# Optimization experiments

Hardware: AMD Instinct MI355X
Metric: run time of the kernel (lower is better)

## Reference

```python
import jax, jax.numpy as jnp
import numpy as np

N = 50000
E = 800000
D = 128
L = 2


def setup_inputs() -> dict:
    key = jax.random.key(0)
    ks = jax.random.split(key, 8)
    x = jax.random.normal(ks[0], (N, D), dtype=jnp.float32)
    edge_index = jax.random.randint(ks[1], (2, E), 0, N, dtype=jnp.int64)
    s = 1.0 / np.sqrt(D)
    Wl = jax.random.uniform(ks[2], (L, D, D), jnp.float32, -s, s)  # neighbor transform (with bias)
    bl = jax.random.uniform(ks[3], (L, D), jnp.float32, -s, s)
    Wr = jax.random.uniform(ks[4], (L, D, D), jnp.float32, -s, s)  # root/self transform (no bias)
    W = jax.random.uniform(ks[5], (D, D), jnp.float32, -s, s)      # final Linear
    b = jax.random.uniform(ks[6], (D,), jnp.float32, -s, s)
    return {"x": x, "edge_index": edge_index, "Wl": Wl, "bl": bl, "Wr": Wr, "W": W, "b": b}


def reference(x, edge_index, Wl, bl, Wr, W, b):
    src, dst = edge_index[0], edge_index[1]
    n = x.shape[0]
    for l in range(Wl.shape[0]):
        # gather neighbor (source) features, scatter-max into destination nodes
        agg = jax.ops.segment_max(x[src], dst, num_segments=n)  # [N, D]
        agg = jnp.where(jnp.isneginf(agg), 0.0, agg)  # PyG: isolated nodes -> 0
        # SAGEConv: lin_l(agg) + lin_r(x)
        x = agg @ Wl[l].T + bl[l] + x @ Wr[l].T
        x = jax.nn.relu(x)
    return x @ W.T + b
```

## Files before the change

### kernel.cpp

```cpp
#include <hip/hip_runtime.h>
#include <math.h>

#define NN 50000
#define NE 800000
#define DD 128
#define NBUCK 196
#define PTILE 4096
#define PBLOCKS 196
#define CONVB 6250

typedef unsigned short u16;
typedef short s8v __attribute__((ext_vector_type(8)));
typedef float f16v __attribute__((ext_vector_type(16)));

__device__ __forceinline__ u16 f2bf(float f) {
    unsigned u = __float_as_uint(f);
    return (u16)((u + 0x7FFFu + ((u >> 16) & 1u)) >> 16);
}
__device__ __forceinline__ float bflo(unsigned u) { return __uint_as_float(u << 16); }
__device__ __forceinline__ float bfhi(unsigned u) { return __uint_as_float(u & 0xFFFF0000u); }

__device__ __forceinline__ void pack_one(const float* __restrict__ Wl,
                                         const float* __restrict__ Wr,
                                         bool two, int o, u16* __restrict__ out) {
    int j = o & 7;
    int l = (o >> 3) & 63;
    int cn = o >> 9;
    int n = cn & 3;
    int c = cn >> 2;
    int colj = n * 32 + (l & 31);
    int k = c * 16 + (l >> 5) * 8 + j;
    float v;
    if (two) v = (k < DD) ? Wl[colj * DD + k] : Wr[colj * DD + (k - DD)];
    else     v = Wl[colj * DD + k];
    out[o] = f2bf(v);
}

__global__ __launch_bounds__(256) void prep_kernel(
        const float4* __restrict__ x4, ushort4* __restrict__ hb0,
        const float* __restrict__ Wl, const float* __restrict__ Wr,
        const float* __restrict__ W,
        u16* __restrict__ Bpk0, u16* __restrict__ Bpk1, u16* __restrict__ Bpkf,
        int* __restrict__ bcnt) {
    int bid = blockIdx.x;
    int tid = threadIdx.x;
    if (bid < CONVB) {
        int i = bid * 256 + tid;
        float4 v = x4[i];
        ushort4 o;
        o.x = f2bf(v.x); o.y = f2bf(v.y); o.z = f2bf(v.z); o.w = f2bf(v.w);
        hb0[i] = o;
    } else if (bid < CONVB + 128) {
        pack_one(Wl, Wr, true, (bid - CONVB) * 256 + tid, Bpk0);
    } else if (bid < CONVB + 256) {
        pack_one(Wl + DD * DD, Wr + DD * DD, true, (bid - CONVB - 128) * 256 + tid, Bpk1);
    } else if (bid < CONVB + 320) {
        pack_one(W, W, false, (bid - CONVB - 256) * 256 + tid, Bpkf);
    } else {
        if (tid < NBUCK) bcnt[tid] = 0;
    }
}

__global__ __launch_bounds__(256) void bucket_hist(const int* __restrict__ ei,
                                                   int* __restrict__ bcnt) {
    __shared__ int h[NBUCK];
    for (int i = threadIdx.x; i < NBUCK; i += 256) h[i] = 0;
    __syncthreads();
    int e0 = blockIdx.x * PTILE;
#pragma unroll
    for (int i = 0; i < 16; i++) {
        int e = e0 + i * 256 + threadIdx.x;
        if (e < NE) atomicAdd(&h[ei[NE + e] >> 8], 1);
    }
    __syncthreads();
    for (int i = threadIdx.x; i < NBUCK; i += 256)
        if (h[i]) atomicAdd(&bcnt[i], h[i]);
}

__global__ __launch_bounds__(256) void bucket_scan(const int* __restrict__ bcnt,
                                                   int* __restrict__ bbase,
                                                   int* __restrict__ bcur,
                                                   int* __restrict__ rowptr) {
    __shared__ int s[256];
    int t = threadIdx.x;
    int v = (t < NBUCK) ? bcnt[t] : 0;
    s[t] = v;
    __syncthreads();
    for (int o = 1; o < 256; o <<= 1) {
        int u = (t >= o) ? s[t - o] : 0;
        __syncthreads();
        s[t] += u;
        __syncthreads();
    }
    int ex = s[t] - v;
    if (t < NBUCK) { bbase[t] = ex; bcur[t] = ex; }
    if (t == 0) rowptr[NN] = NE;
}

__global__ __launch_bounds__(256) void bucket_partition(const int* __restrict__ ei,
                                                        int* __restrict__ bcur,
                                                        unsigned* __restrict__ packed) {
    __shared__ int h[NBUCK];
    __shared__ int base[NBUCK];
    int t = threadIdx.x;
    for (int i = t; i < NBUCK; i += 256) h[i] = 0;
    __syncthreads();
    int e0 = blockIdx.x * PTILE;
    int dsts[16], srcs[16];
#pragma unroll
    for (int i = 0; i < 16; i++) {
        int e = e0 + i * 256 + t;
        if (e < NE) {
            dsts[i] = ei[NE + e];
            srcs[i] = ei[e];
            atomicAdd(&h[dsts[i] >> 8], 1);
        } else dsts[i] = -1;
    }
    __syncthreads();
    for (int i = t; i < NBUCK; i += 256) {
        int c = h[i];
        base[i] = c ? atomicAdd(&bcur[i], c) : 0;
    }
    __syncthreads();
    for (int i = t; i < NBUCK; i += 256) h[i] = 0;
    __syncthreads();
#pragma unroll
    for (int i = 0; i < 16; i++) {
        if (dsts[i] >= 0) {
            int bk = dsts[i] >> 8;
            int r = atomicAdd(&h[bk], 1);
            packed[base[bk] + r] = (unsigned)srcs[i] | ((unsigned)(dsts[i] & 255) << 16);
        }
    }
}

__global__ __launch_bounds__(256) void bucket_csr(const unsigned* __restrict__ packed,
                                                  const int* __restrict__ bcnt,
                                                  const int* __restrict__ bbase,
                                                  int* __restrict__ rowptr,
                                                  int* __restrict__ col) {
    __shared__ int deg[256];
    __shared__ int off[256];
    int bk = blockIdx.x;
    int cnt = bcnt[bk], base = bbase[bk];
    int t = threadIdx.x;
    deg[t] = 0;
    __syncthreads();
    for (int i = t; i < cnt; i += 256) atomicAdd(&deg[packed[base + i] >> 16], 1);
    __syncthreads();
    int v = deg[t];
    off[t] = v;
    __syncthreads();
    for (int o = 1; o < 256; o <<= 1) {
        int u = (t >= o) ? off[t - o] : 0;
        __syncthreads();
        off[t] += u;
        __syncthreads();
    }
    int ex = off[t] - v;
    int node = (bk << 8) + t;
    if (node < NN) rowptr[node] = base + ex;
    deg[t] = ex;
    __syncthreads();
    for (int i = t; i < cnt; i += 256) {
        unsigned p = packed[base + i];
        int dl = p >> 16;
        int r = atomicAdd(&deg[dl], 1);
        col[base + r] = (int)(p & 0xFFFFu);
    }
}

__device__ __forceinline__ void vmax8(float* m, uint4 v) {
    m[0] = fmaxf(m[0], bflo(v.x)); m[1] = fmaxf(m[1], bfhi(v.x));
    m[2] = fmaxf(m[2], bflo(v.y)); m[3] = fmaxf(m[3], bfhi(v.y));
    m[4] = fmaxf(m[4], bflo(v.z)); m[5] = fmaxf(m[5], bfhi(v.z));
    m[6] = fmaxf(m[6], bflo(v.w)); m[7] = fmaxf(m[7], bfhi(v.w));
}

__global__ __launch_bounds__(256) void agg_kernel_bf(const uint4* __restrict__ xb4,
                                                     const int* __restrict__ row_ptr,
                                                     const int* __restrict__ col,
                                                     uint4* __restrict__ aggb4) {
    int node = blockIdx.x * 16 + (threadIdx.x >> 4);
    if (node >= NN) return;
    int j = threadIdx.x & 15;
    int s0 = row_ptr[node], s1 = row_ptr[node + 1];
    if (s0 == s1) {
        aggb4[(size_t)node * 16 + j] = make_uint4(0, 0, 0, 0);
        return;
    }
    float m0[8], m1[8], m2[8], m3[8];
#pragma unroll
    for (int q = 0; q < 8; q++) { m0[q] = m1[q] = m2[q] = m3[q] = -INFINITY; }
    int i = s0;
    for (; i + 8 <= s1; i += 8) {
        int c0 = col[i],     c1 = col[i + 1], c2 = col[i + 2], c3 = col[i + 3];
        int c4 = col[i + 4], c5 = col[i + 5], c6 = col[i + 6], c7 = col[i + 7];
        uint4 v0 = xb4[(size_t)c0 * 16 + j];
        uint4 v1 = xb4[(size_t)c1 * 16 + j];
        uint4 v2 = xb4[(size_t)c2 * 16 + j];
        uint4 v3 = xb4[(size_t)c3 * 16 + j];
        uint4 v4 = xb4[(size_t)c4 * 16 + j];
        uint4 v5 = xb4[(size_t)c5 * 16 + j];
        uint4 v6 = xb4[(size_t)c6 * 16 + j];
        uint4 v7 = xb4[(size_t)c7 * 16 + j];
        vmax8(m0, v0); vmax8(m1, v1); vmax8(m2, v2); vmax8(m3, v3);
        vmax8(m0, v4); vmax8(m1, v5); vmax8(m2, v6); vmax8(m3, v7);
    }
    for (; i + 4 <= s1; i += 4) {
        int c0 = col[i], c1 = col[i + 1], c2 = col[i + 2], c3 = col[i + 3];
        uint4 v0 = xb4[(size_t)c0 * 16 + j];
        uint4 v1 = xb4[(size_t)c1 * 16 + j];
        uint4 v2 = xb4[(size_t)c2 * 16 + j];
        uint4 v3 = xb4[(size_t)c3 * 16 + j];
        vmax8(m0, v0); vmax8(m1, v1); vmax8(m2, v2); vmax8(m3, v3);
    }
    for (; i < s1; i++) {
        uint4 v = xb4[(size_t)col[i] * 16 + j];
        vmax8(m0, v);
    }
#pragma unroll
    for (int q = 0; q < 8; q++) m0[q] = fmaxf(fmaxf(m0[q], m1[q]), fmaxf(m2[q], m3[q]));
    uint4 o;
    o.x = (__float_as_uint(m0[0]) >> 16) | (__float_as_uint(m0[1]) & 0xFFFF0000u);
    o.y = (__float_as_uint(m0[2]) >> 16) | (__float_as_uint(m0[3]) & 0xFFFF0000u);
    o.z = (__float_as_uint(m0[4]) >> 16) | (__float_as_uint(m0[5]) & 0xFFFF0000u);
    o.w = (__float_as_uint(m0[6]) >> 16) | (__float_as_uint(m0[7]) & 0xFFFF0000u);
    aggb4[(size_t)node * 16 + j] = o;
}

template<int NKC16, bool TWO_SRC, bool RELU, bool OUT_BF16>
__global__ __launch_bounds__(256) void mfma_gemm(const u16* __restrict__ srcA,
                                                 const u16* __restrict__ srcB,
                                                 const u16* __restrict__ Bpk,
                                                 const float* __restrict__ bias,
                                                 void* __restrict__ outv) {
    int tid = threadIdx.x;
    int wt = tid >> 6;
    int lane = tid & 63;
    int row0 = blockIdx.x * 128 + wt * 32;
    int rload = row0 + (lane & 31);
    if (rload > NN - 1) rload = NN - 1;
    int koff = (lane >> 5) * 8;
    const s8v* Bv = (const s8v*)Bpk;

    f16v acc[4];
#pragma unroll
    for (int n = 0; n < 4; n++) acc[n] = (f16v)(0.0f);

#pragma unroll
    for (int c = 0; c < NKC16; c++) {
        const u16* s = srcA;
        int kk = c * 16;
        if (TWO_SRC && c >= 8) { s = srcB; kk = (c - 8) * 16; }
        s8v a = *(const s8v*)(s + (size_t)rload * DD + kk + koff);
#pragma unroll
        for (int n = 0; n < 4; n++) {
            s8v b = Bv[(c * 4 + n) * 64 + lane];
            acc[n] = __builtin_amdgcn_mfma_f32_32x32x16_bf16(a, b, acc[n], 0, 0, 0);
        }
    }

    int rowadd = 4 * (lane >> 5);
#pragma unroll
    for (int n = 0; n < 4; n++) {
        int colj = n * 32 + (lane & 31);
        float bj = bias[colj];
#pragma unroll
        for (int r = 0; r < 16; r++) {
            int row = row0 + (r & 3) + 8 * (r >> 2) + rowadd;
            if (row < NN) {
                float v = acc[n][r] + bj;
                if (RELU) v = fmaxf(v, 0.0f);
                if (OUT_BF16) ((u16*)outv)[(size_t)row * DD + colj] = f2bf(v);
                else          ((float*)outv)[(size_t)row * DD + colj] = v;
            }
        }
    }
}

extern "C" void kernel_launch(void* const* d_in, const int* in_sizes, int n_in,
                              void* d_out, int out_size, void* d_ws, size_t ws_size,
                              hipStream_t stream) {
    const float* x  = (const float*)d_in[0];
    const int*   ei = (const int*)d_in[1];
    const float* Wl = (const float*)d_in[2];
    const float* bl = (const float*)d_in[3];
    const float* Wr = (const float*)d_in[4];
    const float* W  = (const float*)d_in[5];
    const float* b  = (const float*)d_in[6];
    float* out = (float*)d_out;

    u16* aggb = (u16*)d_ws;
    u16* hb0  = aggb + (size_t)NN * DD;
    u16* hb1  = hb0 + (size_t)NN * DD;
    u16* Bpk0 = hb1 + (size_t)NN * DD;
    u16* Bpk1 = Bpk0 + 32768;
    u16* Bpkf = Bpk1 + 32768;
    unsigned* packed = (unsigned*)(Bpkf + 16384);
    int* col    = (int*)(packed + NE);
    int* rowptr = col + NE;
    int* bcnt   = rowptr + NN + 1;
    int* bbase  = bcnt + NBUCK;
    int* bcur   = bbase + NBUCK;

    dim3 blk(256);
    int gemmBlocks = (NN + 127) / 128;
    int aggBlocks  = (NN + 15) / 16;
    int prepBlocks = CONVB + 320 + 1;

    prep_kernel<<<prepBlocks, blk, 0, stream>>>(
        (const float4*)x, (ushort4*)hb0, Wl, Wr, W, Bpk0, Bpk1, Bpkf, bcnt);

    bucket_hist<<<PBLOCKS, blk, 0, stream>>>(ei, bcnt);
    bucket_scan<<<1, blk, 0, stream>>>(bcnt, bbase, bcur, rowptr);
    bucket_partition<<<PBLOCKS, blk, 0, stream>>>(ei, bcur, packed);
    bucket_csr<<<NBUCK, blk, 0, stream>>>(packed, bcnt, bbase, rowptr, col);

    agg_kernel_bf<<<aggBlocks, blk, 0, stream>>>((const uint4*)hb0, rowptr, col, (uint4*)aggb);
    mfma_gemm<16, true, true, true><<<gemmBlocks, blk, 0, stream>>>(
        aggb, hb0, Bpk0, bl, hb1);

    agg_kernel_bf<<<aggBlocks, blk, 0, stream>>>((const uint4*)hb1, rowptr, col, (uint4*)aggb);
    mfma_gemm<16, true, true, true><<<gemmBlocks, blk, 0, stream>>>(
        aggb, hb1, Bpk1, bl + DD, hb0);

    mfma_gemm<8, false, false, false><<<gemmBlocks, blk, 0, stream>>>(
        hb0, nullptr, Bpkf, b, out);
}
```

Measured before the change: 241.6 us.

## Fuse bucket histogram into prep, use per-block offsets, slice aggregation by feature

Bucket histogramming moves into the prep kernel and writes per-block counts to a [bucket][block] table, which removes one launch. The single-block scan now also computes per-block exclusive offsets, so partition needs no global atomics and no second pass over its edges. The aggregation kernel splits the 16 feature chunks into 4 slices across blocks, with 4 threads per node and 64 nodes per block, to raise parallelism and per-node memory-level concurrency. The costs are a serial 196-iteration loop per thread in the single-block scan and redundant row_ptr/col reads across the slices.

```diff
diff --git a/kernel.cpp b/kernel.cpp
--- a/kernel.cpp
+++ b/kernel.cpp
@@ -8,6 +8,8 @@
 #define PTILE 4096
 #define PBLOCKS 196
 #define CONVB 6250
+#define ASLICE 4
+#define ABLK 782
 
 typedef unsigned short u16;
 typedef short s8v __attribute__((ext_vector_type(8)));
@@ -37,54 +39,50 @@
 }
 
 __global__ __launch_bounds__(256) void prep_kernel(
+        const int* __restrict__ ei, int* __restrict__ part,
         const float4* __restrict__ x4, ushort4* __restrict__ hb0,
         const float* __restrict__ Wl, const float* __restrict__ Wr,
         const float* __restrict__ W,
-        u16* __restrict__ Bpk0, u16* __restrict__ Bpk1, u16* __restrict__ Bpkf,
-        int* __restrict__ bcnt) {
+        u16* __restrict__ Bpk0, u16* __restrict__ Bpk1, u16* __restrict__ Bpkf) {
     int bid = blockIdx.x;
     int tid = threadIdx.x;
-    if (bid < CONVB) {
-        int i = bid * 256 + tid;
+    if (bid < PBLOCKS) {
+        __shared__ int h[NBUCK];
+        for (int i = tid; i < NBUCK; i += 256) h[i] = 0;
+        __syncthreads();
+        int e0 = bid * PTILE;
+#pragma unroll
+        for (int i = 0; i < 16; i++) {
+            int e = e0 + i * 256 + tid;
+            if (e < NE) atomicAdd(&h[ei[NE + e] >> 8], 1);
+        }
+        __syncthreads();
+        for (int i = tid; i < NBUCK; i += 256) part[i * 256 + bid] = h[i];
+    } else if (bid < PBLOCKS + CONVB) {
+        int i = (bid - PBLOCKS) * 256 + tid;
         float4 v = x4[i];
         ushort4 o;
         o.x = f2bf(v.x); o.y = f2bf(v.y); o.z = f2bf(v.z); o.w = f2bf(v.w);
         hb0[i] = o;
-    } else if (bid < CONVB + 128) {
-        pack_one(Wl, Wr, true, (bid - CONVB) * 256 + tid, Bpk0);
-    } else if (bid < CONVB + 256) {
-        pack_one(Wl + DD * DD, Wr + DD * DD, true, (bid - CONVB - 128) * 256 + tid, Bpk1);
-    } else if (bid < CONVB + 320) {
-        pack_one(W, W, false, (bid - CONVB - 256) * 256 + tid, Bpkf);
+    } else if (bid < PBLOCKS + CONVB + 128) {
+        pack_one(Wl, Wr, true, (bid - PBLOCKS - CONVB) * 256 + tid, Bpk0);
+    } else if (bid < PBLOCKS + CONVB + 256) {
+        pack_one(Wl + DD * DD, Wr + DD * DD, true, (bid - PBLOCKS - CONVB - 128) * 256 + tid, Bpk1);
     } else {
-        if (tid < NBUCK) bcnt[tid] = 0;
-    }
-}
-
-__global__ __launch_bounds__(256) void bucket_hist(const int* __restrict__ ei,
-                                                   int* __restrict__ bcnt) {
-    __shared__ int h[NBUCK];
-    for (int i = threadIdx.x; i < NBUCK; i += 256) h[i] = 0;
-    __syncthreads();
-    int e0 = blockIdx.x * PTILE;
-#pragma unroll
-    for (int i = 0; i < 16; i++) {
-        int e = e0 + i * 256 + threadIdx.x;
-        if (e < NE) atomicAdd(&h[ei[NE + e] >> 8], 1);
-    }
-    __syncthreads();
-    for (int i = threadIdx.x; i < NBUCK; i += 256)
-        if (h[i]) atomicAdd(&bcnt[i], h[i]);
-}
-
-__global__ __launch_bounds__(256) void bucket_scan(const int* __restrict__ bcnt,
+        pack_one(W, W, false, (bid - PBLOCKS - CONVB - 256) * 256 + tid, Bpkf);
+    }
+}
+
+__global__ __launch_bounds__(256) void bucket_scan(int* __restrict__ part,
+                                                   int* __restrict__ bcnt,
                                                    int* __restrict__ bbase,
-                                                   int* __restrict__ bcur,
                                                    int* __restrict__ rowptr) {
     __shared__ int s[256];
     int t = threadIdx.x;
-    int v = (t < NBUCK) ? bcnt[t] : 0;
-    s[t] = v;
+    int tot = 0;
+    if (t < NBUCK)
+        for (int b = 0; b < PBLOCKS; b++) tot += part[t * 256 + b];
+    s[t] = tot;
     __syncthreads();
     for (int o = 1; o < 256; o <<= 1) {
         int u = (t >= o) ? s[t - o] : 0;
@@ -92,44 +90,42 @@
         s[t] += u;
         __syncthreads();
     }
-    int ex = s[t] - v;
-    if (t < NBUCK) { bbase[t] = ex; bcur[t] = ex; }
+    int ex = s[t] - tot;
+    if (t < NBUCK) {
+        bcnt[t] = tot;
+        bbase[t] = ex;
+        int run = ex;
+        for (int b = 0; b < PBLOCKS; b++) {
+            int c = part[t * 256 + b];
+            part[t * 256 + b] = run;
+            run += c;
+        }
+    }
     if (t == 0) rowptr[NN] = NE;
 }
 
 __global__ __launch_bounds__(256) void bucket_partition(const int* __restrict__ ei,
-                                                        int* __restrict__ bcur,
+                                                        const int* __restrict__ part,
                                                         unsigned* __restrict__ packed) {
     __shared__ int h[NBUCK];
     __shared__ int base[NBUCK];
     int t = threadIdx.x;
-    for (int i = t; i < NBUCK; i += 256) h[i] = 0;
-    __syncthreads();
-    int e0 = blockIdx.x * PTILE;
-    int dsts[16], srcs[16];
+    int blk = blockIdx.x;
+    for (int i = t; i < NBUCK; i += 256) {
+        base[i] = part[i * 256 + blk];
+        h[i] = 0;
+    }
+    __syncthreads();
+    int e0 = blk * PTILE;
 #pragma unroll
     for (int i = 0; i < 16; i++) {
         int e = e0 + i * 256 + t;
         if (e < NE) {
-            dsts[i] = ei[NE + e];
-            srcs[i] = ei[e];
-            atomicAdd(&h[dsts[i] >> 8], 1);
-        } else dsts[i] = -1;
-    }
-    __syncthreads();
-    for (int i = t; i < NBUCK; i += 256) {
-        int c = h[i];
-        base[i] = c ? atomicAdd(&bcur[i], c) : 0;
-    }
-    __syncthreads();
-    for (int i = t; i < NBUCK; i += 256) h[i] = 0;
-    __syncthreads();
-#pragma unroll
-    for (int i = 0; i < 16; i++) {
-        if (dsts[i] >= 0) {
-            int bk = dsts[i] >> 8;
+            int dst = ei[NE + e];
+            int src = ei[e];
+            int bk = dst >> 8;
             int r = atomicAdd(&h[bk], 1);
-            packed[base[bk] + r] = (unsigned)srcs[i] | ((unsigned)(dsts[i] & 255) << 16);
+            packed[base[bk] + r] = (unsigned)src | ((unsigned)(dst & 255) << 16);
         }
     }
 }
@@ -181,9 +177,12 @@
                                                      const int* __restrict__ row_ptr,
                                                      const int* __restrict__ col,
                                                      uint4* __restrict__ aggb4) {
-    int node = blockIdx.x * 16 + (threadIdx.x >> 4);
+    int bid = blockIdx.x;
+    int slice = bid / ABLK;
+    int blk = bid - slice * ABLK;
+    int node = blk * 64 + (threadIdx.x >> 2);
     if (node >= NN) return;
-    int j = threadIdx.x & 15;
+    int j = (threadIdx.x & 3) + slice * 4;
     int s0 = row_ptr[node], s1 = row_ptr[node + 1];
     if (s0 == s1) {
         aggb4[(size_t)node * 16 + j] = make_uint4(0, 0, 0, 0);
@@ -302,19 +301,18 @@
     int* rowptr = col + NE;
     int* bcnt   = rowptr + NN + 1;
     int* bbase  = bcnt + NBUCK;
-    int* bcur   = bbase + NBUCK;
+    int* part   = bbase + NBUCK;
 
     dim3 blk(256);
     int gemmBlocks = (NN + 127) / 128;
-    int aggBlocks  = (NN + 15) / 16;
-    int prepBlocks = CONVB + 320 + 1;
+    int aggBlocks  = ASLICE * ABLK;
+    int prepBlocks = PBLOCKS + CONVB + 320;
 
     prep_kernel<<<prepBlocks, blk, 0, stream>>>(
-        (const float4*)x, (ushort4*)hb0, Wl, Wr, W, Bpk0, Bpk1, Bpkf, bcnt);
-
-    bucket_hist<<<PBLOCKS, blk, 0, stream>>>(ei, bcnt);
-    bucket_scan<<<1, blk, 0, stream>>>(bcnt, bbase, bcur, rowptr);
-    bucket_partition<<<PBLOCKS, blk, 0, stream>>>(ei, bcur, packed);
+        ei, part, (const float4*)x, (ushort4*)hb0, Wl, Wr, W, Bpk0, Bpk1, Bpkf);
+
+    bucket_scan<<<1, blk, 0, stream>>>(part, bcnt, bbase, rowptr);
+    bucket_partition<<<PBLOCKS, blk, 0, stream>>>(ei, part, packed);
     bucket_csr<<<NBUCK, blk, 0, stream>>>(packed, bcnt, bbase, rowptr, col);
 
     agg_kernel_bf<<<aggBlocks, blk, 0, stream>>>((const uint4*)hb0, rowptr, col, (uint4*)aggb);
```

After: 269.3 us. 1.11x slower.

## Fuse histogram into prep, degree-sort aggregation nodes, fuse last GEMMs

Applied to the files above, without the earlier changes.

Folds the bucket histogram into the prep kernel and zeroes the counts with a memset, which removes one launch. bucket_csr now builds a per-bucket permutation that orders nodes by degree, so the 16-lane groups in one aggregation block get similar workloads and less divergence. The second SAGE GEMM and the final Linear are fused through LDS, which avoids writing and re-reading the last hidden layer in global memory. The cost is an extra perm lookup per aggregation group and heavier LDS use in the fused GEMM, which may reduce occupancy.

```diff
diff --git a/kernel.cpp b/kernel.cpp
--- a/kernel.cpp
+++ b/kernel.cpp
@@ -8,6 +8,7 @@
 #define PTILE 4096
 #define PBLOCKS 196
 #define CONVB 6250
+#define LHS 136
 
 typedef unsigned short u16;
 typedef short s8v __attribute__((ext_vector_type(8)));
@@ -37,44 +38,39 @@
 }
 
 __global__ __launch_bounds__(256) void prep_kernel(
-        const float4* __restrict__ x4, ushort4* __restrict__ hb0,
+        const int* __restrict__ ei, int* __restrict__ bcnt,
+        const float4* __restrict__ x4, ushort4* __restrict__ hbx,
         const float* __restrict__ Wl, const float* __restrict__ Wr,
         const float* __restrict__ W,
-        u16* __restrict__ Bpk0, u16* __restrict__ Bpk1, u16* __restrict__ Bpkf,
-        int* __restrict__ bcnt) {
+        u16* __restrict__ Bpk0, u16* __restrict__ Bpk1, u16* __restrict__ Bpkf) {
     int bid = blockIdx.x;
     int tid = threadIdx.x;
-    if (bid < CONVB) {
-        int i = bid * 256 + tid;
+    if (bid < PBLOCKS) {
+        __shared__ int h[NBUCK];
+        for (int i = tid; i < NBUCK; i += 256) h[i] = 0;
+        __syncthreads();
+        int e0 = bid * PTILE;
+#pragma unroll
+        for (int i = 0; i < 16; i++) {
+            int e = e0 + i * 256 + tid;
+            if (e < NE) atomicAdd(&h[ei[NE + e] >> 8], 1);
+        }
+        __syncthreads();
+        for (int i = tid; i < NBUCK; i += 256)
+            if (h[i]) atomicAdd(&bcnt[i], h[i]);
+    } else if (bid < PBLOCKS + CONVB) {
+        int i = (bid - PBLOCKS) * 256 + tid;
         float4 v = x4[i];
         ushort4 o;
         o.x = f2bf(v.x); o.y = f2bf(v.y); o.z = f2bf(v.z); o.w = f2bf(v.w);
-        hb0[i] = o;
-    } else if (bid < CONVB + 128) {
-        pack_one(Wl, Wr, true, (bid - CONVB) * 256 + tid, Bpk0);
-    } else if (bid < CONVB + 256) {
-        pack_one(Wl + DD * DD, Wr + DD * DD, true, (bid - CONVB - 128) * 256 + tid, Bpk1);
-    } else if (bid < CONVB + 320) {
-        pack_one(W, W, false, (bid - CONVB - 256) * 256 + tid, Bpkf);
+        hbx[i] = o;
+    } else if (bid < PBLOCKS + CONVB + 128) {
+        pack_one(Wl, Wr, true, (bid - PBLOCKS - CONVB) * 256 + tid, Bpk0);
+    } else if (bid < PBLOCKS + CONVB + 256) {
+        pack_one(Wl + DD * DD, Wr + DD * DD, true, (bid - PBLOCKS - CONVB - 128) * 256 + tid, Bpk1);
     } else {
-        if (tid < NBUCK) bcnt[tid] = 0;
-    }
-}
-
-__global__ __launch_bounds__(256) void bucket_hist(const int* __restrict__ ei,
-                                                   int* __restrict__ bcnt) {
-    __shared__ int h[NBUCK];
-    for (int i = threadIdx.x; i < NBUCK; i += 256) h[i] = 0;
-    __syncthreads();
-    int e0 = blockIdx.x * PTILE;
-#pragma unroll
-    for (int i = 0; i < 16; i++) {
-        int e = e0 + i * 256 + threadIdx.x;
-        if (e < NE) atomicAdd(&h[ei[NE + e] >> 8], 1);
-    }
-    __syncthreads();
-    for (int i = threadIdx.x; i < NBUCK; i += 256)
-        if (h[i]) atomicAdd(&bcnt[i], h[i]);
+        pack_one(W, W, false, (bid - PBLOCKS - CONVB - 256) * 256 + tid, Bpkf);
+    }
 }
 
 __global__ __launch_bounds__(256) void bucket_scan(const int* __restrict__ bcnt,
@@ -138,13 +134,17 @@
                                                   const int* __restrict__ bcnt,
                                                   const int* __restrict__ bbase,
                                                   int* __restrict__ rowptr,
-                                                  int* __restrict__ col) {
+                                                  int* __restrict__ col,
+                                                  int* __restrict__ perm) {
     __shared__ int deg[256];
     __shared__ int off[256];
+    __shared__ int dh[64];
+    __shared__ int ds64[64];
     int bk = blockIdx.x;
     int cnt = bcnt[bk], base = bbase[bk];
     int t = threadIdx.x;
     deg[t] = 0;
+    if (t < 64) dh[t] = 0;
     __syncthreads();
     for (int i = t; i < cnt; i += 256) atomicAdd(&deg[packed[base + i] >> 16], 1);
     __syncthreads();
@@ -159,8 +159,11 @@
     }
     int ex = off[t] - v;
     int node = (bk << 8) + t;
-    if (node < NN) rowptr[node] = base + ex;
+    bool valid = node < NN;
+    if (valid) rowptr[node] = base + ex;
     deg[t] = ex;
+    int dcl = valid ? min(v, 63) : 0;
+    int rank = atomicAdd(&dh[dcl], 1);
     __syncthreads();
     for (int i = t; i < cnt; i += 256) {
         unsigned p = packed[base + i];
@@ -168,6 +171,16 @@
         int r = atomicAdd(&deg[dl], 1);
         col[base + r] = (int)(p & 0xFFFFu);
     }
+    if (t < 64) ds64[t] = dh[t];
+    __syncthreads();
+    for (int o = 1; o < 64; o <<= 1) {
+        int u = (t >= o && t < 64) ? ds64[t - o] : 0;
+        __syncthreads();
+        if (t < 64) ds64[t] += u;
+        __syncthreads();
+    }
+    int pos = ds64[dcl] - dh[dcl] + rank;
+    perm[(bk << 8) + pos] = node;
 }
 
 __device__ __forceinline__ void vmax8(float* m, uint4 v) {
@@ -180,8 +193,10 @@
 __global__ __launch_bounds__(256) void agg_kernel_bf(const uint4* __restrict__ xb4,
                                                      const int* __restrict__ row_ptr,
                                                      const int* __restrict__ col,
+                                                     const int* __restrict__ perm,
                                                      uint4* __restrict__ aggb4) {
-    int node = blockIdx.x * 16 + (threadIdx.x >> 4);
+    int slot = blockIdx.x * 16 + (threadIdx.x >> 4);
+    int node = perm[slot];
     if (node >= NN) return;
     int j = threadIdx.x & 15;
     int s0 = row_ptr[node], s1 = row_ptr[node + 1];
@@ -229,12 +244,11 @@
     aggb4[(size_t)node * 16 + j] = o;
 }
 
-template<int NKC16, bool TWO_SRC, bool RELU, bool OUT_BF16>
-__global__ __launch_bounds__(256) void mfma_gemm(const u16* __restrict__ srcA,
-                                                 const u16* __restrict__ srcB,
-                                                 const u16* __restrict__ Bpk,
-                                                 const float* __restrict__ bias,
-                                                 void* __restrict__ outv) {
+__global__ __launch_bounds__(256) void mfma_gemm0(const u16* __restrict__ srcA,
+                                                  const u16* __restrict__ srcB,
+                                                  const u16* __restrict__ Bpk,
+                                                  const float* __restrict__ bias,
+                                                  u16* __restrict__ outb) {
     int tid = threadIdx.x;
     int wt = tid >> 6;
     int lane = tid & 63;
@@ -249,10 +263,9 @@
     for (int n = 0; n < 4; n++) acc[n] = (f16v)(0.0f);
 
 #pragma unroll
-    for (int c = 0; c < NKC16; c++) {
-        const u16* s = srcA;
-        int kk = c * 16;
-        if (TWO_SRC && c >= 8) { s = srcB; kk = (c - 8) * 16; }
+    for (int c = 0; c < 16; c++) {
+        const u16* s = (c >= 8) ? srcB : srcA;
+        int kk = (c >= 8) ? (c - 8) * 16 : c * 16;
         s8v a = *(const s8v*)(s + (size_t)rload * DD + kk + koff);
 #pragma unroll
         for (int n = 0; n < 4; n++) {
@@ -269,12 +282,80 @@
 #pragma unroll
         for (int r = 0; r < 16; r++) {
             int row = row0 + (r & 3) + 8 * (r >> 2) + rowadd;
-            if (row < NN) {
-                float v = acc[n][r] + bj;
-                if (RELU) v = fmaxf(v, 0.0f);
-                if (OUT_BF16) ((u16*)outv)[(size_t)row * DD + colj] = f2bf(v);
-                else          ((float*)outv)[(size_t)row * DD + colj] = v;
-            }
+            if (row < NN) outb[(size_t)row * DD + colj] = f2bf(fmaxf(acc[n][r] + bj, 0.0f));
+        }
+    }
+}
+
+__global__ __launch_bounds__(256) void mfma_gemm1_final(const u16* __restrict__ srcA,
+                                                        const u16* __restrict__ srcB,
+                                                        const u16* __restrict__ Bpk1,
+                                                        const float* __restrict__ bias1,
+                                                        const u16* __restrict__ Bpkf,
+                                                        const float* __restrict__ bias2,
+                                                        float* __restrict__ out) {
+    __shared__ u16 lh[128 * LHS];
+    int tid = threadIdx.x;
+    int wt = tid >> 6;
+    int lane = tid & 63;
+    int row0 = blockIdx.x * 128 + wt * 32;
+    int rload = row0 + (lane & 31);
+    if (rload > NN - 1) rload = NN - 1;
+    int koff = (lane >> 5) * 8;
+    const s8v* Bv1 = (const s8v*)Bpk1;
+    const s8v* Bvf = (const s8v*)Bpkf;
+
+    f16v acc[4];
+#pragma unroll
+    for (int n = 0; n < 4; n++) acc[n] = (f16v)(0.0f);
+
+#pragma unroll
+    for (int c = 0; c < 16; c++) {
+        const u16* s = (c >= 8) ? srcB : srcA;
+        int kk = (c >= 8) ? (c - 8) * 16 : c * 16;
+        s8v a = *(const s8v*)(s + (size_t)rload * DD + kk + koff);
+#pragma unroll
+        for (int n = 0; n < 4; n++) {
+            s8v b = Bv1[(c * 4 + n) * 64 + lane];
+            acc[n] = __builtin_amdgcn_mfma_f32_32x32x16_bf16(a, b, acc[n], 0, 0, 0);
+        }
+    }
+
+    int rowadd = 4 * (lane >> 5);
+#pragma unroll
+    for (int n = 0; n < 4; n++) {
+        int colj = n * 32 + (lane & 31);
+        float bj = bias1[colj];
+#pragma unroll
+        for (int r = 0; r < 16; r++) {
+            int rl = (r & 3) + 8 * (r >> 2) + rowadd;
+            lh[(wt * 32 + rl) * LHS + colj] = f2bf(fmaxf(acc[n][r] + bj, 0.0f));
+        }
+    }
+    __syncthreads();
+
+    f16v acc2[4];
+#pragma unroll
+    for (int n = 0; n < 4; n++) acc2[n] = (f16v)(0.0f);
+    int m = lane & 31;
+#pragma unroll
+    for (int c = 0; c < 8; c++) {
+        s8v a = *(const s8v*)&lh[(wt * 32 + m) * LHS + c * 16 + koff];
+#pragma unroll
+        for (int n = 0; n < 4; n++) {
+            s8v b = Bvf[(c * 4 + n) * 64 + lane];
+            acc2[n] = __builtin_amdgcn_mfma_f32_32x32x16_bf16(a, b, acc2[n], 0, 0, 0);
+        }
+    }
+
+#pragma unroll
+    for (int n = 0; n < 4; n++) {
+        int colj = n * 32 + (lane & 31);
+        float bj = bias2[colj];
+#pragma unroll
+        for (int r = 0; r < 16; r++) {
+            int row = row0 + (r & 3) + 8 * (r >> 2) + rowadd;
+            if (row < NN) out[(size_t)row * DD + colj] = acc2[n][r] + bj;
         }
     }
 }
@@ -292,39 +373,36 @@
     float* out = (float*)d_out;
 
     u16* aggb = (u16*)d_ws;
-    u16* hb0  = aggb + (size_t)NN * DD;
-    u16* hb1  = hb0 + (size_t)NN * DD;
-    u16* Bpk0 = hb1 + (size_t)NN * DD;
+    u16* hbx  = aggb + (size_t)NN * DD;
+    u16* h1   = hbx + (size_t)NN * DD;
+    u16* Bpk0 = h1 + (size_t)NN * DD;
     u16* Bpk1 = Bpk0 + 32768;
     u16* Bpkf = Bpk1 + 32768;
     unsigned* packed = (unsigned*)(Bpkf + 16384);
     int* col    = (int*)(packed + NE);
     int* rowptr = col + NE;
-    int* bcnt   = rowptr + NN + 1;
+    int* perm   = rowptr + NN + 1;
+    int* bcnt   = perm + NBUCK * 256;
     int* bbase  = bcnt + NBUCK;
     int* bcur   = bbase + NBUCK;
 
     dim3 blk(256);
     int gemmBlocks = (NN + 127) / 128;
-    int aggBlocks  = (NN + 15) / 16;
-    int prepBlocks = CONVB + 320 + 1;
+    int aggBlocks  = NBUCK * 256 / 16;
+    int prepBlocks = PBLOCKS + CONVB + 320;
+
+    hipMemsetAsync(bcnt, 0, NBUCK * sizeof(int), stream);
 
     prep_kernel<<<prepBlocks, blk, 0, stream>>>(
-        (const float4*)x, (ushort4*)hb0, Wl, Wr, W, Bpk0, Bpk1, Bpkf, bcnt);
-
-    bucket_hist<<<PBLOCKS, blk, 0, stream>>>(ei, bcnt);
+        ei, bcnt, (const float4*)x, (ushort4*)hbx, Wl, Wr, W, Bpk0, Bpk1, Bpkf);
+
     bucket_scan<<<1, blk, 0, stream>>>(bcnt, bbase, bcur, rowptr);
     bucket_partition<<<PBLOCKS, blk, 0, stream>>>(ei, bcur, packed);
-    bucket_csr<<<NBUCK, blk, 0, stream>>>(packed, bcnt, bbase, rowptr, col);
-
-    agg_kernel_bf<<<aggBlocks, blk, 0, stream>>>((const uint4*)hb0, rowptr, col, (uint4*)aggb);
-    mfma_gemm<16, true, true, true><<<gemmBlocks, blk, 0, stream>>>(
-        aggb, hb0, Bpk0, bl, hb1);
-
-    agg_kernel_bf<<<aggBlocks, blk, 0, stream>>>((const uint4*)hb1, rowptr, col, (uint4*)aggb);
-    mfma_gemm<16, true, true, true><<<gemmBlocks, blk, 0, stream>>>(
-        aggb, hb1, Bpk1, bl + DD, hb0);
-
-    mfma_gemm<8, false, false, false><<<gemmBlocks, blk, 0, stream>>>(
-        hb0, nullptr, Bpkf, b, out);
-}
+    bucket_csr<<<NBUCK, blk, 0, stream>>>(packed, bcnt, bbase, rowptr, col, perm);
+
+    agg_kernel_bf<<<aggBlocks, blk, 0, stream>>>((const uint4*)hbx, rowptr, col, perm, (uint4*)aggb);
+    mfma_gemm0<<<gemmBlocks, blk, 0, stream>>>(aggb, hbx, Bpk0, bl, h1);
+
+    agg_kernel_bf<<<aggBlocks, blk, 0, stream>>>((const uint4*)h1, rowptr, col, perm, (uint4*)aggb);
+    mfma_gemm1_final<<<gemmBlocks, blk, 0, stream>>>(aggb, h1, Bpk1, bl + DD, Bpkf, b, out);
+}
```

Result: slower. 253.1 us (+4.8%).
